# Kernel tuning notes

Measured on AMD Instinct MI355X. Metric: run time of the kernel, lower is better.

## Reference

```python
import jax, jax.numpy as jnp
import numpy as np

TOP_K = 2
POOL = 4  # EfficientSpatialRouter.pool_scale


def silu(v):
    return v * jax.nn.sigmoid(v)


def setup_inputs() -> dict:
    key = jax.random.key(0)
    ks = jax.random.split(key, 6)
    B, C, H, W = 16, 256, 56, 56
    E, O = 4, 256
    hidden = 2 * C            # SimpleExpert expand_ratio=2
    red = max(C // 8, 8)      # router reduced_channels
    x = jax.random.normal(ks[0], (B, C, H, W), jnp.float32)
    router_w1 = jax.random.normal(ks[1], (red, C, 3, 3), jnp.float32) * 0.02
    router_w2 = jax.random.normal(ks[2], (E, red), jnp.float32) * 0.01
    expert_w1 = jax.random.normal(ks[3], (E, hidden, C), jnp.float32) * 0.05
    expert_w2 = jax.random.normal(ks[4], (E, O, hidden), jnp.float32) * 0.03
    shared_w = jax.random.normal(ks[5], (O, C), jnp.float32) * 0.05
    return {"x": x, "router_w1": router_w1, "router_w2": router_w2,
            "expert_w1": expert_w1, "expert_w2": expert_w2, "shared_w": shared_w}


def reference(x, router_w1, router_w2, expert_w1, expert_w2, shared_w):
    # Eval mode: no router noise; BatchNorm with default running stats
    # (mean=0, var=1, gamma=1, beta=0) is the identity, so BNs are omitted.
    B, C, H, W = x.shape
    E = router_w2.shape[0]

    # --- EfficientSpatialRouter ---
    xp = x.reshape(B, C, H // POOL, POOL, W // POOL, POOL).mean(axis=(3, 5))
    h = jax.lax.conv_general_dilated(
        xp, router_w1, window_strides=(1, 1), padding=((1, 1), (1, 1)),
        dimension_numbers=("NCHW", "OIHW", "NCHW"))
    h = silu(h)  # [B, red, H/4, W/4]
    # 1x1 conv to E channels then spatial mean == mean of per-pixel logits
    logits = jnp.einsum("er,brij->be", router_w2, h) / (h.shape[2] * h.shape[3])
    probs = jax.nn.softmax(logits, axis=1)
    topv, topi = jax.lax.top_k(probs, TOP_K)          # [B,k]
    topv = topv / (topv.sum(axis=1, keepdims=True) + 1e-6)

    # --- shared expert (1x1 conv + BN(id) + SiLU) ---
    shared = silu(jnp.einsum("oc,bcij->boij", shared_w, x))

    # --- all SimpleExperts densely (1x1 conv -> SiLU -> 1x1 conv) ---
    hid = silu(jnp.einsum("edc,bcij->bedij", expert_w1, x))   # [B,E,hid,H,W]
    eo = jnp.einsum("eod,bedij->beoij", expert_w2, hid)       # [B,E,O,H,W]

    # --- weighted combine of top-k experts ---
    wdense = jnp.zeros((B, E), x.dtype).at[jnp.arange(B)[:, None], topi].add(topv)
    expert_out = jnp.einsum("be,beoij->boij", wdense, eo)
    return shared + expert_out
```

## Files before the change

kernel.cpp:

```cpp
#include <hip/hip_runtime.h>
#include <hip/hip_bf16.h>

typedef __attribute__((ext_vector_type(8))) short bf16x8;
typedef __attribute__((ext_vector_type(16))) float f32x16;
typedef __attribute__((ext_vector_type(4))) unsigned short ushort4v;

static __device__ __forceinline__ unsigned short f2bf(float f) {
  unsigned u = __float_as_uint(f);
  return (unsigned short)((u + 0x7FFFu + ((u >> 16) & 1u)) >> 16);
}
static __device__ __forceinline__ float silu_f(float v) { return v / (1.f + __expf(-v)); }

#define MFMA32(a, b, c) __builtin_amdgcn_mfma_f32_32x32x16_bf16((a), (b), (c), 0, 0, 0)
#define SBAR() __builtin_amdgcn_sched_barrier(0x102)

__global__ void prep_k(const float* __restrict__ shw, const float* __restrict__ ew1,
                       const float* __restrict__ ew2, const float* __restrict__ x,
                       unsigned short* __restrict__ wshp, unsigned short* __restrict__ w1p,
                       unsigned short* __restrict__ w2p, float* __restrict__ xp) {
  const int bid = blockIdx.x;
  if (bid < 4352) {
    int idx = bid * 256 + threadIdx.x;
    if (idx < 65536) {
      int j = idx;
      int i = j & 7, l = (j >> 3) & 63, ks = (j >> 9) & 15, rb = j >> 13;
      int row = rb * 32 + (l & 31), k = ks * 16 + (l >> 5) * 8 + i;
      wshp[j] = f2bf(shw[row * 256 + k]);
    } else if (idx < 589824) {
      int j = idx - 65536;
      int i = j & 7, l = (j >> 3) & 63, ks = (j >> 9) & 15, rb = (j >> 13) & 15, e = j >> 17;
      int row = rb * 32 + (l & 31), k = ks * 16 + (l >> 5) * 8 + i;
      w1p[j] = f2bf(ew1[((size_t)e * 512 + row) * 256 + k]);
    } else if (idx < 1114112) {
      int j = idx - 589824;
      int i = j & 7, l = (j >> 3) & 63, ks = (j >> 9) & 31, rb = (j >> 14) & 7, e = j >> 17;
      int row = rb * 32 + (l & 31), k = ks * 16 + (l >> 5) * 8 + i;
      w2p[j] = f2bf(ew2[((size_t)e * 256 + row) * 512 + k]);
    }
  } else {
    int idx = (bid - 4352) * 256 + threadIdx.x;
    if (idx >= 16 * 256 * 196) return;
    int pj = idx % 14, tmp = idx / 14, pi = tmp % 14, bc = tmp / 14;
    const float* src = x + (size_t)bc * 3136 + pi * 4 * 56 + pj * 4;
    float s = 0.f;
#pragma unroll
    for (int u = 0; u < 4; ++u) {
      float4 v = *reinterpret_cast<const float4*>(src + u * 56);
      s += v.x + v.y + v.z + v.w;
    }
    xp[idx] = s * 0.0625f;
  }
}

__global__ __launch_bounds__(256) void router_conv_k(const float* __restrict__ xp,
                                                     const float* __restrict__ rw1,
                                                     float* __restrict__ hsum) {
  const int b = blockIdx.x >> 5, r = blockIdx.x & 31;
  __shared__ float wl[2304];
  __shared__ float xl[32][256];
  __shared__ float red[4];
  const int t = threadIdx.x;
  for (int i = t; i < 2304; i += 256) wl[i] = rw1[r * 2304 + i];
  for (int i = t; i < 32 * 256; i += 256) (&xl[0][0])[i] = 0.f;
  const int pi = t / 14, pj = t % 14;
  float acc = 0.f;
  for (int cc = 0; cc < 8; ++cc) {
    __syncthreads();
    for (int i = t; i < 32 * 196; i += 256) {
      int c = i / 196, px = i % 196;
      xl[c][(px / 14 + 1) * 16 + (px % 14 + 1)] =
          xp[((size_t)b * 256 + cc * 32 + c) * 196 + px];
    }
    __syncthreads();
    if (t < 196) {
      for (int c = 0; c < 32; ++c) {
        const float* wp = &wl[(cc * 32 + c) * 9];
        const float* xc = &xl[c][pi * 16 + pj];
#pragma unroll
        for (int u = 0; u < 3; ++u)
#pragma unroll
          for (int v = 0; v < 3; ++v) acc += xc[u * 16 + v] * wp[u * 3 + v];
      }
    }
  }
  float s = (t < 196) ? silu_f(acc) : 0.f;
#pragma unroll
  for (int off = 32; off > 0; off >>= 1) s += __shfl_down(s, off);
  if ((t & 63) == 0) red[t >> 6] = s;
  __syncthreads();
  if (t == 0) hsum[b * 32 + r] = red[0] + red[1] + red[2] + red[3];
}

__global__ void topk_k(const float* __restrict__ hsum, const float* __restrict__ rw2,
                       float* __restrict__ selv, int* __restrict__ sele) {
  const int t = threadIdx.x;
  const int b = t >> 2, e = t & 3;
  float l = 0.f;
#pragma unroll
  for (int r = 0; r < 32; ++r) l += rw2[e * 32 + r] * hsum[b * 32 + r];
  l *= (1.f / 196.f);
  float m = fmaxf(l, __shfl_xor(l, 1));
  m = fmaxf(m, __shfl_xor(m, 2));
  float p = __expf(l - m);
  float sm = p + __shfl_xor(p, 1);
  sm += __shfl_xor(sm, 2);
  float prob = p / sm;
  float p0 = __shfl(prob, (b << 2) | 0);
  float p1 = __shfl(prob, (b << 2) | 1);
  float p2 = __shfl(prob, (b << 2) | 2);
  float p3 = __shfl(prob, (b << 2) | 3);
  if (e == 0) {
    float pr[4] = {p0, p1, p2, p3};
    int i1 = 0;
    for (int i = 1; i < 4; ++i)
      if (pr[i] > pr[i1]) i1 = i;
    int i2 = (i1 == 0) ? 1 : 0;
    for (int i = 0; i < 4; ++i) {
      if (i == i1 || i == i2) continue;
      if (pr[i] > pr[i2]) i2 = i;
    }
    float denom = pr[i1] + pr[i2] + 1e-6f;
    selv[b * 2 + 0] = pr[i1] / denom;
    selv[b * 2 + 1] = pr[i2] / denom;
    sele[b * 2 + 0] = i1;
    sele[b * 2 + 1] = i2;
  }
}

__global__ __launch_bounds__(512, 4) void moe_main_k(
    const float* __restrict__ x, const unsigned short* __restrict__ wshp,
    const unsigned short* __restrict__ w1p, const unsigned short* __restrict__ w2p,
    const float* __restrict__ selv, const int* __restrict__ sele,
    float* __restrict__ out) {
  constexpr int HW = 3136;
  __shared__ __align__(16) unsigned short xs[32 * 64 * 8];
  __shared__ __align__(16) unsigned short hs[2][16 * 64 * 8];

  const int b = blockIdx.x / 49, tile = blockIdx.x - b * 49;
  const int px0 = tile * 64;
  const int t = threadIdx.x;
  const int w = t >> 6, l = t & 63;
  const int l31 = l & 31, lh = l >> 5;

  {
    const float* xb = x + (size_t)b * 256 * HW + px0 + l;
#pragma unroll
    for (int cg = 0; cg < 4; ++cg) {
      const int c0 = w * 32 + cg * 8;
      alignas(16) unsigned short tmp[8];
#pragma unroll
      for (int i = 0; i < 8; ++i) tmp[i] = f2bf(xb[(size_t)(c0 + i) * HW]);
      *reinterpret_cast<bf16x8*>(&xs[((c0 >> 3) * 64 + l) * 8]) =
          *reinterpret_cast<const bf16x8*>(tmp);
    }
  }

  const int e0 = sele[b * 2 + 0], e1 = sele[b * 2 + 1];
  const float v0 = selv[b * 2 + 0], v1 = selv[b * 2 + 1];

  const unsigned short* xB0 = xs + (lh * 64 + l31) * 8;
  const unsigned short* xB1 = xB0 + 256;

  __syncthreads();

  if (w < 4) {
    f32x16 hacc[2];
#pragma unroll 1
    for (int q = 0; q < 8; ++q) {
      const int p = q;
      const int e = (p >> 2) ? e1 : e0, ch = p & 3;
      const float v = (p >> 2) ? v1 : v0;
      const unsigned short* A1 =
          w1p + (size_t)((e * 16 + ch * 4 + w) * 16) * 512 + l * 8;
#pragma unroll
      for (int j = 0; j < 2; ++j)
#pragma unroll
        for (int r = 0; r < 16; ++r) hacc[j][r] = 0.f;
      bf16x8 af[16];
#pragma unroll
      for (int j = 0; j < 16; ++j)
        af[j] = *reinterpret_cast<const bf16x8*>(A1 + j * 512);
      SBAR();
      __builtin_amdgcn_s_setprio(1);
#pragma unroll
      for (int j = 0; j < 16; ++j) {
        const bf16x8 b0 = *reinterpret_cast<const bf16x8*>(xB0 + j * 1024);
        const bf16x8 b1 = *reinterpret_cast<const bf16x8*>(xB1 + j * 1024);
        hacc[0] = MFMA32(af[j], b0, hacc[0]);
        hacc[1] = MFMA32(af[j], b1, hacc[1]);
      }
      __builtin_amdgcn_s_setprio(0);
      ushort4v pk[2][4];
#pragma unroll
      for (int cf = 0; cf < 2; ++cf)
#pragma unroll
        for (int g = 0; g < 4; ++g) {
          alignas(8) unsigned short tmp[4];
#pragma unroll
          for (int j = 0; j < 4; ++j) tmp[j] = f2bf(v * silu_f(hacc[cf][g * 4 + j]));
          pk[cf][g] = *reinterpret_cast<const ushort4v*>(tmp);
        }
#pragma unroll
      for (int cf = 0; cf < 2; ++cf)
#pragma unroll
        for (int g = 0; g < 4; ++g) {
          const int ui2 = ((w * 4 + g) * 64 + cf * 32 + l31) * 8 + lh * 4;
          *reinterpret_cast<ushort4v*>(&hs[p & 1][ui2]) = pk[cf][g];
        }
      __syncthreads();
    }
    __syncthreads();
  } else {
    const int wc = w - 4;
    f32x16 oacc[2][2];
#pragma unroll
    for (int i = 0; i < 2; ++i)
#pragma unroll
      for (int j = 0; j < 2; ++j)
#pragma unroll
        for (int r = 0; r < 16; ++r) oacc[i][j][r] = 0.f;

    {
      const unsigned short* As = wshp + (size_t)(wc * 2) * 16 * 512 + l * 8;
#pragma unroll
      for (int g = 0; g < 4; ++g) {
        bf16x8 a0f[4], a1f[4];
#pragma unroll
        for (int j = 0; j < 4; ++j) {
          a0f[j] = *reinterpret_cast<const bf16x8*>(As + (g * 4 + j) * 512);
          a1f[j] = *reinterpret_cast<const bf16x8*>(As + 8192 + (g * 4 + j) * 512);
        }
        SBAR();
        __builtin_amdgcn_s_setprio(1);
#pragma unroll
        for (int j = 0; j < 4; ++j) {
          const bf16x8 b0 = *reinterpret_cast<const bf16x8*>(xB0 + (g * 4 + j) * 1024);
          const bf16x8 b1 = *reinterpret_cast<const bf16x8*>(xB1 + (g * 4 + j) * 1024);
          oacc[0][0] = MFMA32(a0f[j], b0, oacc[0][0]);
          oacc[0][1] = MFMA32(a0f[j], b1, oacc[0][1]);
          oacc[1][0] = MFMA32(a1f[j], b0, oacc[1][0]);
          oacc[1][1] = MFMA32(a1f[j], b1, oacc[1][1]);
        }
        __builtin_amdgcn_s_setprio(0);
      }
    }
#pragma unroll
    for (int i = 0; i < 2; ++i)
#pragma unroll
      for (int j = 0; j < 2; ++j)
#pragma unroll
        for (int r = 0; r < 16; ++r) oacc[i][j][r] = silu_f(oacc[i][j][r]);

    __syncthreads();
#pragma unroll 1
    for (int q = 0; q < 8; ++q) {
      const int e = (q >> 2) ? e1 : e0, ch = q & 3;
      const unsigned short* A2 =
          w2p + ((size_t)(e * 8 + wc * 2) * 32 + ch * 8) * 512 + l * 8;
      const unsigned short* hB0 = hs[q & 1] + (lh * 64 + l31) * 8;
      const unsigned short* hB1 = hB0 + 256;
#pragma unroll
      for (int g = 0; g < 2; ++g) {
        bf16x8 a0f[4], a1f[4];
#pragma unroll
        for (int j = 0; j < 4; ++j) {
          a0f[j] = *reinterpret_cast<const bf16x8*>(A2 + (g * 4 + j) * 512);
          a1f[j] = *reinterpret_cast<const bf16x8*>(A2 + 16384 + (g * 4 + j) * 512);
        }
        SBAR();
        __builtin_amdgcn_s_setprio(1);
#pragma unroll
        for (int j = 0; j < 4; ++j) {
          const bf16x8 h0 = *reinterpret_cast<const bf16x8*>(hB0 + (g * 4 + j) * 1024);
          const bf16x8 h1 = *reinterpret_cast<const bf16x8*>(hB1 + (g * 4 + j) * 1024);
          oacc[0][0] = MFMA32(a0f[j], h0, oacc[0][0]);
          oacc[0][1] = MFMA32(a0f[j], h1, oacc[0][1]);
          oacc[1][0] = MFMA32(a1f[j], h0, oacc[1][0]);
          oacc[1][1] = MFMA32(a1f[j], h1, oacc[1][1]);
        }
        __builtin_amdgcn_s_setprio(0);
      }
      __syncthreads();
    }

#pragma unroll
    for (int rfi = 0; rfi < 2; ++rfi)
#pragma unroll
      for (int cf = 0; cf < 2; ++cf)
#pragma unroll
        for (int r = 0; r < 16; ++r) {
          const int o = wc * 64 + rfi * 32 + (r & 3) + 8 * (r >> 2) + 4 * lh;
          out[((size_t)b * 256 + o) * HW + px0 + cf * 32 + l31] = oacc[rfi][cf][r];
        }
  }
}

extern "C" void kernel_launch(void* const* d_in, const int* in_sizes, int n_in,
                              void* d_out, int out_size, void* d_ws, size_t ws_size,
                              hipStream_t stream) {
  const float* x = (const float*)d_in[0];
  const float* rw1 = (const float*)d_in[1];
  const float* rw2 = (const float*)d_in[2];
  const float* ew1 = (const float*)d_in[3];
  const float* ew2 = (const float*)d_in[4];
  const float* shw = (const float*)d_in[5];
  float* out = (float*)d_out;
  char* ws = (char*)d_ws;

  float* xp = (float*)(ws);
  float* hsum = (float*)(ws + 3211264);
  float* selv = (float*)(ws + 3213312);
  int* sele = (int*)(ws + 3213440);
  unsigned short* wshp = (unsigned short*)(ws + 3213568);
  unsigned short* w1p = wshp + 65536;
  unsigned short* w2p = w1p + 524288;

  prep_k<<<7488, 256, 0, stream>>>(shw, ew1, ew2, x, wshp, w1p, w2p, xp);
  router_conv_k<<<512, 256, 0, stream>>>(xp, rw1, hsum);
  topk_k<<<1, 64, 0, stream>>>(hsum, rw2, selv, sele);
  moe_main_k<<<784, 512, 0, stream>>>(x, wshp, w1p, w2p, selv, sele, out);
}
```

Baseline: 169.4 us.

## Double-buffer expert weight fragments across phases and register-tile router conv

The main MoE kernel now prefetches the next phase's expert weight fragments into a second register buffer while the current phase's MFMAs run, in both the producer and consumer warps. Block-wide sync is replaced by a custom barrier that waits only on LDS counters, so outstanding global loads can stay in flight across it. Occupancy hint drops from 4 to 2 blocks per CU to make room for the doubled register buffers. The router conv also changes so each thread computes a 2x2 output patch over a channel slice, followed by an LDS reduction. The cost is higher register pressure and lower occupancy. Prefetching phase p+1 on the last iteration reads past the selected expert's weights, which looks like an out-of-range read.

```diff
diff --git a/kernel.cpp b/kernel.cpp
--- a/kernel.cpp
+++ b/kernel.cpp
@@ -12,7 +12,14 @@
 static __device__ __forceinline__ float silu_f(float v) { return v / (1.f + __expf(-v)); }
 
 #define MFMA32(a, b, c) __builtin_amdgcn_mfma_f32_32x32x16_bf16((a), (b), (c), 0, 0, 0)
-#define SBAR() __builtin_amdgcn_sched_barrier(0x102)
+
+#define PHASE_BARRIER()                                   \
+  do {                                                    \
+    asm volatile("s_waitcnt lgkmcnt(0)" ::: "memory");    \
+    __builtin_amdgcn_sched_barrier(0);                    \
+    __builtin_amdgcn_s_barrier();                         \
+    __builtin_amdgcn_sched_barrier(0);                    \
+  } while (0)
 
 __global__ void prep_k(const float* __restrict__ shw, const float* __restrict__ ew1,
                        const float* __restrict__ ew2, const float* __restrict__ x,
@@ -58,12 +65,14 @@
   const int b = blockIdx.x >> 5, r = blockIdx.x & 31;
   __shared__ float wl[2304];
   __shared__ float xl[32][256];
-  __shared__ float red[4];
+  __shared__ float red[4][196];
+  __shared__ float red2[4];
   const int t = threadIdx.x;
+  const int w = t >> 6, l = t & 63;
   for (int i = t; i < 2304; i += 256) wl[i] = rw1[r * 2304 + i];
   for (int i = t; i < 32 * 256; i += 256) (&xl[0][0])[i] = 0.f;
-  const int pi = t / 14, pj = t % 14;
-  float acc = 0.f;
+  const int ui = (l < 49) ? (l / 7) : 0, uj = (l < 49) ? (l % 7) : 0;
+  float acc[4] = {0.f, 0.f, 0.f, 0.f};
   for (int cc = 0; cc < 8; ++cc) {
     __syncthreads();
     for (int i = t; i < 32 * 196; i += 256) {
@@ -72,23 +81,50 @@
           xp[((size_t)b * 256 + cc * 32 + c) * 196 + px];
     }
     __syncthreads();
-    if (t < 196) {
-      for (int c = 0; c < 32; ++c) {
+    if (l < 49) {
+#pragma unroll 2
+      for (int ci = 0; ci < 8; ++ci) {
+        const int c = w * 8 + ci;
+        float xv[4][4];
+        const float* xb = &xl[c][ui * 32 + uj * 2];
+#pragma unroll
+        for (int dr = 0; dr < 4; ++dr)
+#pragma unroll
+          for (int dc = 0; dc < 4; ++dc) xv[dr][dc] = xb[dr * 16 + dc];
         const float* wp = &wl[(cc * 32 + c) * 9];
-        const float* xc = &xl[c][pi * 16 + pj];
-#pragma unroll
-        for (int u = 0; u < 3; ++u)
-#pragma unroll
-          for (int v = 0; v < 3; ++v) acc += xc[u * 16 + v] * wp[u * 3 + v];
+        float wv[9];
+#pragma unroll
+        for (int j = 0; j < 9; ++j) wv[j] = wp[j];
+#pragma unroll
+        for (int di = 0; di < 2; ++di)
+#pragma unroll
+          for (int dj = 0; dj < 2; ++dj) {
+            float a = acc[di * 2 + dj];
+#pragma unroll
+            for (int du = 0; du < 3; ++du)
+#pragma unroll
+              for (int dv = 0; dv < 3; ++dv)
+                a += xv[di + du][dj + dv] * wv[du * 3 + dv];
+            acc[di * 2 + dj] = a;
+          }
       }
     }
   }
-  float s = (t < 196) ? silu_f(acc) : 0.f;
+  if (l < 49) {
+#pragma unroll
+    for (int k = 0; k < 4; ++k) red[w][(ui * 7 + uj) * 4 + k] = acc[k];
+  }
+  __syncthreads();
+  float s = 0.f;
+  if (t < 196) {
+    float tot = red[0][t] + red[1][t] + red[2][t] + red[3][t];
+    s = silu_f(tot);
+  }
 #pragma unroll
   for (int off = 32; off > 0; off >>= 1) s += __shfl_down(s, off);
-  if ((t & 63) == 0) red[t >> 6] = s;
+  if ((t & 63) == 0) red2[t >> 6] = s;
   __syncthreads();
-  if (t == 0) hsum[b * 32 + r] = red[0] + red[1] + red[2] + red[3];
+  if (t == 0) hsum[b * 32 + r] = red2[0] + red2[1] + red2[2] + red2[3];
 }
 
 __global__ void topk_k(const float* __restrict__ hsum, const float* __restrict__ rw2,
@@ -127,7 +163,60 @@
   }
 }
 
-__global__ __launch_bounds__(512, 4) void moe_main_k(
+#define A1PTR(p) (w1p + (size_t)(((((p) >> 2) ? e1 : e0) * 16 + ((p)&3) * 4 + w) * 16) * 512 + l * 8)
+#define A2PTR(q) (w2p + ((size_t)((((q) >> 2) ? e1 : e0) * 8 + wc * 2) * 32 + ((q)&3) * 8) * 512 + l * 8)
+
+#define PRODUCER_PHASE(p, CUR, NXT)                                              \
+  {                                                                              \
+    const unsigned short* A1n = A1PTR((p) + 1);                                  \
+    _Pragma("unroll") for (int j = 0; j < 16; ++j)                               \
+        NXT[j] = *reinterpret_cast<const bf16x8*>(A1n + j * 512);                \
+    const float vv = ((p) >> 2) ? v1 : v0;                                       \
+    _Pragma("unroll") for (int jj = 0; jj < 2; ++jj)                             \
+        _Pragma("unroll") for (int rr = 0; rr < 16; ++rr) hacc[jj][rr] = 0.f;    \
+    __builtin_amdgcn_s_setprio(1);                                               \
+    _Pragma("unroll") for (int kk = 0; kk < 16; ++kk) {                          \
+      const bf16x8 bb0 = *reinterpret_cast<const bf16x8*>(xB0 + kk * 1024);      \
+      const bf16x8 bb1 = *reinterpret_cast<const bf16x8*>(xB1 + kk * 1024);      \
+      hacc[0] = MFMA32(CUR[kk], bb0, hacc[0]);                                   \
+      hacc[1] = MFMA32(CUR[kk], bb1, hacc[1]);                                   \
+    }                                                                            \
+    __builtin_amdgcn_s_setprio(0);                                               \
+    _Pragma("unroll") for (int cf = 0; cf < 2; ++cf)                             \
+        _Pragma("unroll") for (int g = 0; g < 4; ++g) {                          \
+      alignas(8) unsigned short tmp[4];                                          \
+      _Pragma("unroll") for (int j = 0; j < 4; ++j)                              \
+          tmp[j] = f2bf(vv * silu_f(hacc[cf][g * 4 + j]));                       \
+      const int ui2 = ((w * 4 + g) * 64 + cf * 32 + l31) * 8 + lh * 4;           \
+      *reinterpret_cast<ushort4v*>(&hs[(p)&1][ui2]) =                            \
+          *reinterpret_cast<const ushort4v*>(tmp);                               \
+    }                                                                            \
+    PHASE_BARRIER();                                                             \
+  }
+
+#define CONSUMER_PHASE(q, CUR, NXT)                                              \
+  {                                                                              \
+    const unsigned short* A2n = A2PTR((q) + 1);                                  \
+    _Pragma("unroll") for (int j = 0; j < 8; ++j) {                              \
+      NXT[j] = *reinterpret_cast<const bf16x8*>(A2n + j * 512);                  \
+      NXT[8 + j] = *reinterpret_cast<const bf16x8*>(A2n + 16384 + j * 512);      \
+    }                                                                            \
+    const unsigned short* hB0 = hs[(q)&1] + (lh * 64 + l31) * 8;                 \
+    const unsigned short* hB1 = hB0 + 256;                                       \
+    __builtin_amdgcn_s_setprio(1);                                               \
+    _Pragma("unroll") for (int kk = 0; kk < 8; ++kk) {                           \
+      const bf16x8 hh0 = *reinterpret_cast<const bf16x8*>(hB0 + kk * 1024);      \
+      const bf16x8 hh1 = *reinterpret_cast<const bf16x8*>(hB1 + kk * 1024);      \
+      oacc[0][0] = MFMA32(CUR[kk], hh0, oacc[0][0]);                             \
+      oacc[0][1] = MFMA32(CUR[kk], hh1, oacc[0][1]);                             \
+      oacc[1][0] = MFMA32(CUR[8 + kk], hh0, oacc[1][0]);                         \
+      oacc[1][1] = MFMA32(CUR[8 + kk], hh1, oacc[1][1]);                         \
+    }                                                                            \
+    __builtin_amdgcn_s_setprio(0);                                               \
+    PHASE_BARRIER();                                                             \
+  }
+
+__global__ __launch_bounds__(512, 2) void moe_main_k(
     const float* __restrict__ x, const unsigned short* __restrict__ wshp,
     const unsigned short* __restrict__ w1p, const unsigned short* __restrict__ w2p,
     const float* __restrict__ selv, const int* __restrict__ sele,
@@ -165,51 +254,19 @@
 
   if (w < 4) {
     f32x16 hacc[2];
+    bf16x8 afA[16], afB[16];
+    {
+      const unsigned short* A1 = A1PTR(0);
+#pragma unroll
+      for (int j = 0; j < 16; ++j)
+        afA[j] = *reinterpret_cast<const bf16x8*>(A1 + j * 512);
+    }
 #pragma unroll 1
-    for (int q = 0; q < 8; ++q) {
-      const int p = q;
-      const int e = (p >> 2) ? e1 : e0, ch = p & 3;
-      const float v = (p >> 2) ? v1 : v0;
-      const unsigned short* A1 =
-          w1p + (size_t)((e * 16 + ch * 4 + w) * 16) * 512 + l * 8;
-#pragma unroll
-      for (int j = 0; j < 2; ++j)
-#pragma unroll
-        for (int r = 0; r < 16; ++r) hacc[j][r] = 0.f;
-      bf16x8 af[16];
-#pragma unroll
-      for (int j = 0; j < 16; ++j)
-        af[j] = *reinterpret_cast<const bf16x8*>(A1 + j * 512);
-      SBAR();
-      __builtin_amdgcn_s_setprio(1);
-#pragma unroll
-      for (int j = 0; j < 16; ++j) {
-        const bf16x8 b0 = *reinterpret_cast<const bf16x8*>(xB0 + j * 1024);
-        const bf16x8 b1 = *reinterpret_cast<const bf16x8*>(xB1 + j * 1024);
-        hacc[0] = MFMA32(af[j], b0, hacc[0]);
-        hacc[1] = MFMA32(af[j], b1, hacc[1]);
-      }
-      __builtin_amdgcn_s_setprio(0);
-      ushort4v pk[2][4];
-#pragma unroll
-      for (int cf = 0; cf < 2; ++cf)
-#pragma unroll
-        for (int g = 0; g < 4; ++g) {
-          alignas(8) unsigned short tmp[4];
-#pragma unroll
-          for (int j = 0; j < 4; ++j) tmp[j] = f2bf(v * silu_f(hacc[cf][g * 4 + j]));
-          pk[cf][g] = *reinterpret_cast<const ushort4v*>(tmp);
-        }
-#pragma unroll
-      for (int cf = 0; cf < 2; ++cf)
-#pragma unroll
-        for (int g = 0; g < 4; ++g) {
-          const int ui2 = ((w * 4 + g) * 64 + cf * 32 + l31) * 8 + lh * 4;
-          *reinterpret_cast<ushort4v*>(&hs[p & 1][ui2]) = pk[cf][g];
-        }
-      __syncthreads();
-    }
-    __syncthreads();
+    for (int qq = 0; qq < 4; ++qq) {
+      PRODUCER_PHASE(2 * qq + 0, afA, afB)
+      PRODUCER_PHASE(2 * qq + 1, afB, afA)
+    }
+    PHASE_BARRIER();
   } else {
     const int wc = w - 4;
     f32x16 oacc[2][2];
@@ -230,7 +287,6 @@
           a0f[j] = *reinterpret_cast<const bf16x8*>(As + (g * 4 + j) * 512);
           a1f[j] = *reinterpret_cast<const bf16x8*>(As + 8192 + (g * 4 + j) * 512);
         }
-        SBAR();
         __builtin_amdgcn_s_setprio(1);
 #pragma unroll
         for (int j = 0; j < 4; ++j) {
@@ -251,36 +307,20 @@
 #pragma unroll
         for (int r = 0; r < 16; ++r) oacc[i][j][r] = silu_f(oacc[i][j][r]);
 
-    __syncthreads();
+    bf16x8 a2A[16], a2B[16];
+    {
+      const unsigned short* A2 = A2PTR(0);
+#pragma unroll
+      for (int j = 0; j < 8; ++j) {
+        a2A[j] = *reinterpret_cast<const bf16x8*>(A2 + j * 512);
+        a2A[8 + j] = *reinterpret_cast<const bf16x8*>(A2 + 16384 + j * 512);
+      }
+    }
+    PHASE_BARRIER();
 #pragma unroll 1
-    for (int q = 0; q < 8; ++q) {
-      const int e = (q >> 2) ? e1 : e0, ch = q & 3;
-      const unsigned short* A2 =
-          w2p + ((size_t)(e * 8 + wc * 2) * 32 + ch * 8) * 512 + l * 8;
-      const unsigned short* hB0 = hs[q & 1] + (lh * 64 + l31) * 8;
-      const unsigned short* hB1 = hB0 + 256;
-#pragma unroll
-      for (int g = 0; g < 2; ++g) {
-        bf16x8 a0f[4], a1f[4];
-#pragma unroll
-        for (int j = 0; j < 4; ++j) {
-          a0f[j] = *reinterpret_cast<const bf16x8*>(A2 + (g * 4 + j) * 512);
-          a1f[j] = *reinterpret_cast<const bf16x8*>(A2 + 16384 + (g * 4 + j) * 512);
-        }
-        SBAR();
-        __builtin_amdgcn_s_setprio(1);
-#pragma unroll
-        for (int j = 0; j < 4; ++j) {
-          const bf16x8 h0 = *reinterpret_cast<const bf16x8*>(hB0 + (g * 4 + j) * 1024);
-          const bf16x8 h1 = *reinterpret_cast<const bf16x8*>(hB1 + (g * 4 + j) * 1024);
-          oacc[0][0] = MFMA32(a0f[j], h0, oacc[0][0]);
-          oacc[0][1] = MFMA32(a0f[j], h1, oacc[0][1]);
-          oacc[1][0] = MFMA32(a1f[j], h0, oacc[1][0]);
-          oacc[1][1] = MFMA32(a1f[j], h1, oacc[1][1]);
-        }
-        __builtin_amdgcn_s_setprio(0);
-      }
-      __syncthreads();
+    for (int qq = 0; qq < 4; ++qq) {
+      CONSUMER_PHASE(2 * qq + 0, a2A, a2B)
+      CONSUMER_PHASE(2 * qq + 1, a2B, a2A)
     }
 
 #pragma unroll
```

Result: slower. 199.5 us (+17.7%).
